# Kernel optimization log

Measured on AMD Instinct MI355X. Metric: run time of the kernel, lower is better.

Reference implementation:

```python
import jax, jax.numpy as jnp
import numpy as np

V, D, DFF, L, H, N, K, NB, R = 32000, 512, 2048, 4, 8, 64, 8, 32, 64
B, S = 2, 512
DH = D // H


def _layernorm(x, g, b, eps=1e-5):
    m = x.mean(-1, keepdims=True)
    v = ((x - m) ** 2).mean(-1, keepdims=True)
    return (x - m) * jax.lax.rsqrt(v + eps) * g + b


def _forward(input_ids, token_emb, pos_emb, basis_A, basis_emb, recipe,
             Wq, bq, Wk, bk, Wv, bv, Ws, bs, Wup, bup, Wdown, bdown,
             ln1_g, ln1_b, ln2_g, ln2_b, alpha, lnf_g, lnf_b):
    Bc, Sc = input_ids.shape
    x = token_emb[input_ids] + pos_emb[:Sc][None]          # [B,S,D]
    causal = jnp.tril(jnp.ones((Sc, Sc), dtype=bool))
    neg = jnp.asarray(-jnp.inf, x.dtype)
    scale = jnp.asarray(1.0 / np.sqrt(DH), x.dtype)
    for i in range(L):
        rec = recipe[i]                                    # [N,NB]
        neuron_emb = jax.nn.softmax(rec, -1) @ basis_emb   # [N,D] routing embedding
        # ---- SimpleRouter on norm1(x) ----
        n1 = _layernorm(x, ln1_g[i], ln1_b[i])
        q = (n1 @ Wq[i] + bq[i]).reshape(Bc, Sc, H, DH)
        k = (n1 @ Wk[i] + bk[i]).reshape(Bc, Sc, H, DH)
        v = (n1 @ Wv[i] + bv[i]).reshape(Bc, Sc, H, DH)
        attn = jnp.einsum('bqhd,bkhd->bhqk', q, k) * scale
        attn = jnp.where(causal[None, None], attn, neg)
        attn = jax.nn.softmax(attn, -1)
        ctx = jnp.einsum('bhqk,bkhd->bqhd', attn, v).reshape(Bc, Sc, D)
        query = jnp.concatenate([n1, ctx], -1) @ Ws[i] + bs[i]   # [B,S,D]
        scores = query @ neuron_emb.T                            # [B,S,N]
        topk_scores, topk_idx = jax.lax.top_k(scores, K)
        weights = jax.nn.softmax(topk_scores, -1)                # [B,S,K]
        # ---- BasisResidualFFN on norm2(x) ----
        n2 = _layernorm(x, ln2_g[i], ln2_b[i])
        sel = jax.nn.softmax(rec[topk_idx], -1)                  # [B,S,K,NB]
        token_recipe = (sel * weights[..., None]).sum(2)         # [B,S,NB]
        # delta = x @ W_A @ W_A^T with W_A = token_recipe . basis_A, computed
        # WITHOUT materializing [B,S,D,R] (same math, associativity only)
        proj = jnp.einsum('bsd,ndr->bsnr', n2, basis_A)          # [B,S,NB,R]
        h = jnp.einsum('bsn,bsnr->bsr', token_recipe, proj)      # [B,S,R]
        delta = jnp.einsum('bsn,bsr,ndr->bsd', token_recipe, h, basis_A)
        xf = n2 + alpha[i] * delta
        ff = jax.nn.gelu(xf @ Wup[i] + bup[i], approximate=False) @ Wdown[i] + bdown[i]
        x = x + ff                                               # dropout=0 (eval)
    x = _layernorm(x, lnf_g, lnf_b)
    return x @ token_emb.T                                       # tied head


def setup_inputs() -> dict:
    key = jax.random.key(0)
    ks = iter(jax.random.split(key, 40))
    std = 0.02
    nrm = lambda shape, s=std: jax.random.normal(next(ks), shape, jnp.float32) * s
    input_ids = jax.random.randint(next(ks), (B, S), 0, V)
    basis_A = jax.random.normal(next(ks), (NB, D, R), jnp.float32)
    basis_A = basis_A / jnp.linalg.norm(basis_A.reshape(NB, -1), axis=-1)[:, None, None]
    basis_emb = jax.random.normal(next(ks), (NB, D), jnp.float32)
    basis_emb = basis_emb / jnp.linalg.norm(basis_emb, axis=-1, keepdims=True)
    return dict(
        input_ids=input_ids,
        token_emb=nrm((V, D)), pos_emb=nrm((S, D)),
        basis_A=basis_A, basis_emb=basis_emb,
        recipe=jax.random.normal(next(ks), (L, N, NB), jnp.float32) * 0.5,
        Wq=nrm((L, D, D)), bq=jnp.zeros((L, D)),
        Wk=nrm((L, D, D)), bk=jnp.zeros((L, D)),
        Wv=nrm((L, D, D)), bv=jnp.zeros((L, D)),
        Ws=nrm((L, 2 * D, D)), bs=jnp.zeros((L, D)),
        Wup=nrm((L, D, DFF)), bup=jnp.zeros((L, DFF)),
        Wdown=nrm((L, DFF, D)), bdown=jnp.zeros((L, D)),
        ln1_g=jnp.ones((L, D)), ln1_b=jnp.zeros((L, D)),
        ln2_g=jnp.ones((L, D)), ln2_b=jnp.zeros((L, D)),
        alpha=jnp.full((L,), 0.1, jnp.float32),
        lnf_g=jnp.ones((D,)), lnf_b=jnp.zeros((D,)),
    )


def reference(input_ids, token_emb, pos_emb, basis_A, basis_emb, recipe,
              Wq, bq, Wk, bk, Wv, bv, Ws, bs, Wup, bup, Wdown, bdown,
              ln1_g, ln1_b, ln2_g, ln2_b, alpha, lnf_g, lnf_b):
    return _forward(input_ids, token_emb, pos_emb, basis_A, basis_emb, recipe,
                    Wq, bq, Wk, bk, Wv, bv, Ws, bs, Wup, bup, Wdown, bdown,
                    ln1_g, ln1_b, ln2_g, ln2_b, alpha, lnf_g, lnf_b)
```

## Files before the change

### kernel.cpp

```cpp
#include <hip/hip_runtime.h>
#include <hip/hip_bf16.h>
#include <math.h>

#define V_  32000
#define D_  512
#define DFF_ 2048
#define L_  4
#define H_  8
#define N_  64
#define K_  8
#define NB_ 32
#define R_  64
#define B_  2
#define S_  512
#define T_  1024
#define DH_ 64

typedef short bhalf8 __attribute__((ext_vector_type(8)));
typedef float floatx4 __attribute__((ext_vector_type(4)));

#define GLOAD16(gp, lp) __builtin_amdgcn_global_load_lds( \
    (const __attribute__((address_space(1))) void*)(gp), \
    (__attribute__((address_space(3))) void*)(lp), 16, 0, 0)

__device__ __forceinline__ float gelu_f(float v) {
    return 0.5f * v * (1.0f + erff(v * 0.70710678118654752f));
}

__device__ __forceinline__ unsigned pk2(float a, float b) {
    unsigned ua = (unsigned)__bfloat16_as_ushort(__float2bfloat16(a));
    unsigned ub = (unsigned)__bfloat16_as_ushort(__float2bfloat16(b));
    return ua | (ub << 16);
}

template<int BM, int BN, int WR, int WC, int EPI>
__device__ __forceinline__ void gemm_dev(
    short* __restrict__ lds,
    const __hip_bfloat16* __restrict__ A, int lda, long sA,
    const __hip_bfloat16* __restrict__ Bt, int ldb, long sB,
    const float* __restrict__ bias,
    const float* __restrict__ aux,
    void* __restrict__ Cv, int ldc, long sC,
    int Kdim, int bm, int bn, int z)
{
    constexpr int FM = BM / WR / 16;
    constexpr int FN = BN / WC / 16;
    constexpr int ACH = BM * 8;
    constexpr int BCH = BN * 8;
    constexpr int HALF = (BM + BN) * 64;
    A  += (long)z * sA;
    Bt += (long)z * sB;
    const int tid = threadIdx.x;
    const int w = tid >> 6, lane = tid & 63;
    const int wr = w / WC, wc = w % WC;
    const int moff = wr * (BM / WR), noff = wc * (BN / WC);
    floatx4 acc[FM][FN] = {};

    auto stage = [&](int buf, int k0) {
        char* baseA = (char*)(lds + buf * HALF);
        char* baseB = (char*)(lds + buf * HALF + BM * 64);
        #pragma unroll
        for (int i = 0; i < ACH / 256; i++) {
            int c = tid + i * 256;
            int m = c >> 3, u = (c & 7) ^ (m & 7);
            GLOAD16(A + (long)(bm + m) * lda + k0 + u * 8, baseA + (w * 64 + i * 256) * 16);
        }
        #pragma unroll
        for (int i = 0; i < BCH / 256; i++) {
            int c = tid + i * 256;
            int m = c >> 3, u = (c & 7) ^ (m & 7);
            GLOAD16(Bt + (long)(bn + m) * ldb + k0 + u * 8, baseB + (w * 64 + i * 256) * 16);
        }
    };

    const int nt = Kdim >> 6;
    stage(0, 0);
    __syncthreads();
    int cur = 0;
    for (int t = 0; t < nt; ++t) {
        if (t + 1 < nt) stage(cur ^ 1, (t + 1) * 64);
        const char* baseA = (const char*)(lds + cur * HALF);
        const char* baseB = (const char*)(lds + cur * HALF + BM * 64);
        #pragma unroll
        for (int kk = 0; kk < 2; kk++) {
            bhalf8 af[FM], bf[FN];
            #pragma unroll
            for (int fm = 0; fm < FM; fm++) {
                int row = moff + fm * 16 + (lane & 15);
                int u = (kk * 4 + (lane >> 4)) ^ (row & 7);
                af[fm] = *(const bhalf8*)(baseA + row * 128 + u * 16);
            }
            #pragma unroll
            for (int fn = 0; fn < FN; fn++) {
                int row = noff + fn * 16 + (lane & 15);
                int u = (kk * 4 + (lane >> 4)) ^ (row & 7);
                bf[fn] = *(const bhalf8*)(baseB + row * 128 + u * 16);
            }
            #pragma unroll
            for (int fm = 0; fm < FM; fm++)
                #pragma unroll
                for (int fn = 0; fn < FN; fn++)
                    acc[fm][fn] = __builtin_amdgcn_mfma_f32_16x16x32_bf16(
                        af[fm], bf[fn], acc[fm][fn], 0, 0, 0);
        }
        __syncthreads();
        cur ^= 1;
    }

    float* Cf = (float*)Cv;
    __hip_bfloat16* Cb = (__hip_bfloat16*)Cv;
    __hip_bfloat16* vtb = (EPI == 5) ? (__hip_bfloat16*)(void*)aux : nullptr;
    const long zoff = (long)z * sC;
    const int lr = lane >> 4, lc = lane & 15;

    if constexpr (EPI == 7) {
        float* st = (float*)lds;
        #pragma unroll
        for (int fm = 0; fm < FM; fm++)
            #pragma unroll
            for (int fn = 0; fn < FN; fn++)
                #pragma unroll
                for (int i = 0; i < 4; i++)
                    st[(moff + fm * 16 + lr * 4 + i) * 65 + noff + fn * 16 + lc] =
                        acc[fm][fn][i];
        __syncthreads();
        #pragma unroll
        for (int it = 0; it < (BM * BN / 4) / 256; it++) {
            int slot = it * 256 + tid;
            int r = slot >> 4, c4 = (slot & 15) * 4;
            float4 v = *(float4*)&st[r * 65 + c4];
            *(float4*)&Cf[zoff + (long)(bm + r) * ldc + bn + c4] = v;
        }
        __syncthreads();
        return;
    }

    float alphaV = (EPI == 3) ? bias[0] : 0.f;
    #pragma unroll
    for (int fm = 0; fm < FM; fm++) {
        #pragma unroll
        for (int fn = 0; fn < FN; fn++) {
            int cN = bn + noff + fn * 16 + lc;
            float bv = (EPI == 3 || !bias || (EPI == 6 && z != 0)) ? 0.f : bias[cN];
            #pragma unroll
            for (int i = 0; i < 4; i++) {
                int rM = bm + moff + fm * 16 + lr * 4 + i;
                long idx = zoff + (long)rM * ldc + cN;
                float v = acc[fm][fn][i] + bv;
                if constexpr (EPI == 0) Cf[idx] = v;
                else if constexpr (EPI == 1) Cb[idx] = __float2bfloat16(v);
                else if constexpr (EPI == 2) Cb[idx] = __float2bfloat16(gelu_f(v));
                else if constexpr (EPI == 3)
                    Cb[idx] = __float2bfloat16(aux[idx] + alphaV * acc[fm][fn][i]);
                else if constexpr (EPI == 4) Cf[idx] += v;
                else if constexpr (EPI == 5) {
                    __hip_bfloat16 bvv = __float2bfloat16(v);
                    Cb[idx] = bvv;
                    if (cN >= 1024) {
                        int hh = (cN - 1024) >> 6, dh = (cN - 1024) & 63;
                        int bb = rM >> 9, ss = rM & 511;
                        vtb[(((long)bb * 8 + hh) * 64 + dh) * 512 + ss] = bvv;
                    }
                }
                else if constexpr (EPI == 6) atomicAdd(&Cf[idx], v);
            }
        }
    }
}

template<int BM, int BN, int WR, int WC, int EPI, int SWZ = 0>
__global__ __launch_bounds__(256) void gemm_mfma(
    const __hip_bfloat16* __restrict__ A, int lda, long sA,
    const __hip_bfloat16* __restrict__ Bt, int ldb, long sB,
    const float* __restrict__ bias,
    const float* __restrict__ aux,
    void* __restrict__ Cv, int ldc, long sC,
    int Kdim)
{
    __shared__ short lds[2 * (BM + BN) * 64];
    int bm, bn;
    if constexpr (SWZ == 1) {
        constexpr int MT = T_ / BM;
        constexpr int NP = V_ / BN;
        constexpr int PPX = (NP + 7) / 8;
        int d = blockIdx.x;
        int xcd = d & 7, k = d >> 3;
        int ty = xcd * PPX + (k >> 3);
        if (ty >= NP) return;
        bm = (k & (MT - 1)) * BM;
        bn = ty * BN;
    } else {
        bm = blockIdx.y * BM;
        bn = blockIdx.x * BN;
    }
    gemm_dev<BM, BN, WR, WC, EPI>(lds, A, lda, sA, Bt, ldb, sB, bias, aux,
                                  Cv, ldc, sC, Kdim, bm, bn, blockIdx.z);
}

__global__ __launch_bounds__(256) void mega_gemm(
    const __hip_bfloat16* __restrict__ catB, const __hip_bfloat16* __restrict__ qkvT,
    const float* __restrict__ bqkv, __hip_bfloat16* __restrict__ VtB,
    __hip_bfloat16* __restrict__ qkvB,
    const __hip_bfloat16* __restrict__ WsB, const __hip_bfloat16* __restrict__ neB,
    __hip_bfloat16* __restrict__ WsneK,
    const __hip_bfloat16* __restrict__ n2B, const __hip_bfloat16* __restrict__ projT,
    float* __restrict__ P)
{
    __shared__ short lds[2 * 192 * 64];
    int blk = blockIdx.x;
    if (blk < 384) {
        gemm_dev<64, 64, 2, 2, 5>(lds, catB, 1024, 0, qkvT, D_, 0, bqkv,
                                  (const float*)VtB, qkvB, 1536, 0, D_,
                                  (blk / 24) * 64, (blk % 24) * 64, 0);
    } else if (blk < 400) {
        gemm_dev<64, 64, 2, 2, 1>(lds, WsB, D_, 0, neB, D_, 0, nullptr, nullptr,
                                  WsneK, N_, 0, D_, (blk - 384) * 64, 0, 0);
    } else {
        int local = blk - 400;
        gemm_dev<128, 64, 2, 2, 7>(lds, n2B, D_, 0, projT, D_, (long)R_ * D_,
                                   nullptr, nullptr, P, NB_ * R_, R_, D_,
                                   (local & 7) * 128, 0, local >> 3);
    }
}

__global__ __launch_bounds__(256) void attn_mfma(
    const __hip_bfloat16* __restrict__ qkv,
    const __hip_bfloat16* __restrict__ vt,
    __hip_bfloat16* __restrict__ catB)
{
    __shared__ short pbuf[4][16][72];
    const int tid = threadIdx.x;
    const int w = tid >> 6, lane = tid & 63;
    const int g = lane >> 4, ql = lane & 15;
    const int h = blockIdx.y, b = blockIdx.z;
    const int qbase = blockIdx.x * 64 + w * 16;

    const long qrow = ((long)(b * S_ + qbase + ql)) * 1536 + h * DH_;
    bhalf8 qa0 = *(const bhalf8*)(qkv + qrow + g * 8);
    bhalf8 qa1 = *(const bhalf8*)(qkv + qrow + 32 + g * 8);
    const __hip_bfloat16* kB = qkv + 512;
    const __hip_bfloat16* vbase = vt + ((long)(b * H_ + h)) * DH_ * S_;

    floatx4 o[4] = {};
    float m = -INFINITY, ls = 0.f;
    const float SC = 0.125f * 1.44269504088896f;
    const int nblk = blockIdx.x + 1;

    for (int kvb = 0; kvb < nblk; kvb++) {
        const int kb0 = kvb * 64;
        floatx4 st[4];
        #pragma unroll
        for (int t = 0; t < 4; t++) {
            long krow = ((long)(b * S_ + kb0 + t * 16 + ql)) * 1536 + h * DH_;
            bhalf8 ka0 = *(const bhalf8*)(kB + krow + g * 8);
            bhalf8 ka1 = *(const bhalf8*)(kB + krow + 32 + g * 8);
            floatx4 z = {};
            z = __builtin_amdgcn_mfma_f32_16x16x32_bf16(ka0, qa0, z, 0, 0, 0);
            z = __builtin_amdgcn_mfma_f32_16x16x32_bf16(ka1, qa1, z, 0, 0, 0);
            st[t] = z;
        }
        const int q = qbase + ql;
        float p[4][4];
        float m4 = -INFINITY;
        #pragma unroll
        for (int t = 0; t < 4; t++)
            #pragma unroll
            for (int i = 0; i < 4; i++) {
                int kv = kb0 + t * 16 + g * 4 + i;
                float v = (kv <= q) ? st[t][i] * SC : -INFINITY;
                p[t][i] = v; m4 = fmaxf(m4, v);
            }
        m4 = fmaxf(m4, __shfl_xor(m4, 16));
        m4 = fmaxf(m4, __shfl_xor(m4, 32));
        float mnew = fmaxf(m, m4);
        float corr = exp2f(m - mnew);
        m = mnew;
        float lsum = 0.f;
        #pragma unroll
        for (int t = 0; t < 4; t++)
            #pragma unroll
            for (int i = 0; i < 4; i++) {
                float e = exp2f(p[t][i] - mnew);
                p[t][i] = e; lsum += e;
            }
        lsum += __shfl_xor(lsum, 16);
        lsum += __shfl_xor(lsum, 32);
        ls = ls * corr + lsum;
        unsigned* prow = (unsigned*)&pbuf[w][ql][0];
        #pragma unroll
        for (int t = 0; t < 4; t++) {
            prow[t * 8 + g * 2]     = pk2(p[t][0], p[t][1]);
            prow[t * 8 + g * 2 + 1] = pk2(p[t][2], p[t][3]);
        }
        #pragma unroll
        for (int i = 0; i < 4; i++) {
            float c = __shfl(corr, g * 4 + i);
            #pragma unroll
            for (int dt = 0; dt < 4; dt++) o[dt][i] *= c;
        }
        __syncthreads();
        #pragma unroll
        for (int ks = 0; ks < 2; ks++) {
            bhalf8 pa = *(const bhalf8*)&pbuf[w][ql][ks * 32 + g * 8];
            #pragma unroll
            for (int dt = 0; dt < 4; dt++) {
                bhalf8 vb = *(const bhalf8*)(vbase + (long)(dt * 16 + ql) * S_ + kb0 + ks * 32 + g * 8);
                o[dt] = __builtin_amdgcn_mfma_f32_16x16x32_bf16(pa, vb, o[dt], 0, 0, 0);
            }
        }
        __syncthreads();
    }
    const float inv = 1.f / ls;
    #pragma unroll
    for (int i = 0; i < 4; i++) {
        float iv = __shfl(inv, g * 4 + i);
        int trow = b * S_ + qbase + g * 4 + i;
        #pragma unroll
        for (int dt = 0; dt < 4; dt++)
            catB[(long)trow * 1024 + 512 + h * DH_ + dt * 16 + ql] =
                __float2bfloat16(o[dt][i] * iv);
    }
}

__device__ __forceinline__ void tcvt_dev(const float* in, int ldn, long sIn,
                                         __hip_bfloat16* out, int ldk, long sOut,
                                         int bx, int by, int bz, float (*tsh)[33]) {
    in  += (long)bz * sIn;
    out += (long)bz * sOut;
    int k0 = by * 32, n0 = bx * 32;
    int tx = threadIdx.x & 31, ty = threadIdx.x >> 5;
    #pragma unroll
    for (int r = 0; r < 4; r++) tsh[ty * 4 + r][tx] = in[(long)(k0 + ty * 4 + r) * ldn + n0 + tx];
    __syncthreads();
    #pragma unroll
    for (int r = 0; r < 4; r++)
        out[(long)(n0 + ty * 4 + r) * ldk + k0 + tx] = __float2bfloat16(tsh[tx][ty * 4 + r]);
}

__device__ __forceinline__ void cvt8(const float* in, __hip_bfloat16* out, long i) {
    float4 v0 = *(const float4*)(in + i);
    float4 v1 = *(const float4*)(in + i + 4);
    uint4 pkv = make_uint4(pk2(v0.x, v0.y), pk2(v0.z, v0.w),
                           pk2(v1.x, v1.y), pk2(v1.z, v1.w));
    *(uint4*)(out + i) = pkv;
}

__global__ __launch_bounds__(256) void prologue_kernel(
    const float* __restrict__ temb, __hip_bfloat16* __restrict__ tembB,
    const float* __restrict__ basisA, __hip_bfloat16* __restrict__ projT,
    __hip_bfloat16* __restrict__ deltaT,
    const float* __restrict__ bq, const float* __restrict__ bk,
    const float* __restrict__ bv, float* __restrict__ bqkv,
    const float* __restrict__ Wq, const float* __restrict__ Wk,
    const float* __restrict__ Wv, __hip_bfloat16* __restrict__ qkvT,
    const float* __restrict__ Wup, __hip_bfloat16* __restrict__ WupT,
    const float* __restrict__ Wdn, __hip_bfloat16* __restrict__ WdnT,
    const float* __restrict__ Ws, __hip_bfloat16* __restrict__ WsB,
    const int* __restrict__ ids, const float* __restrict__ pemb,
    float* __restrict__ x)
{
    __shared__ float tsh[32][33];
    const int blk = blockIdx.x, tid = threadIdx.x;
    if (blk < 8000) {
        cvt8(temb, tembB, ((long)blk * 256 + tid) * 8);
    } else if (blk < 12096) {
        long i = (long)(blk - 8000) * 256 + tid;
        int r = i & 63; int d = (i >> 6) & 511; int n = i >> 15;
        __hip_bfloat16 v = __float2bfloat16(basisA[i]);
        projT[((long)n * R_ + r) * D_ + d] = v;
        deltaT[(long)d * (NB_ * R_) + n * R_ + r] = v;
    } else if (blk < 12120) {
        int i = (blk - 12096) * 256 + tid;
        int l = i / 1536, j = i % 1536;
        float v = (j < 512) ? bq[l * 512 + j] : (j < 1024) ? bk[l * 512 + j - 512]
                                                           : bv[l * 512 + j - 1024];
        bqkv[i] = v;
    } else if (blk < 13144) {
        int lin = blk - 12120;
        tcvt_dev(Wq, D_, (long)D_ * D_, qkvT, D_, (long)1536 * D_,
                 lin & 15, (lin >> 4) & 15, lin >> 8, tsh);
    } else if (blk < 14168) {
        int lin = blk - 13144;
        tcvt_dev(Wk, D_, (long)D_ * D_, qkvT + 512 * 512, D_, (long)1536 * D_,
                 lin & 15, (lin >> 4) & 15, lin >> 8, tsh);
    } else if (blk < 15192) {
        int lin = blk - 14168;
        tcvt_dev(Wv, D_, (long)D_ * D_, qkvT + 1024 * 512, D_, (long)1536 * D_,
                 lin & 15, (lin >> 4) & 15, lin >> 8, tsh);
    } else if (blk < 19288) {
        int lin = blk - 15192;
        tcvt_dev(Wup, DFF_, (long)D_ * DFF_, WupT, D_, (long)D_ * DFF_,
                 lin & 63, (lin >> 6) & 15, lin >> 10, tsh);
    } else if (blk < 23384) {
        int lin = blk - 19288;
        tcvt_dev(Wdn, D_, (long)DFF_ * D_, WdnT, DFF_, (long)DFF_ * D_,
                 lin & 15, (lin >> 4) & 63, lin >> 10, tsh);
    } else if (blk < 24408) {
        cvt8(Ws, WsB, ((long)(blk - 23384) * 256 + tid) * 8);
    } else {
        int t = blk - 24408;
        int s = t % S_;
        int id = ids[t];
        for (int d = tid; d < D_; d += 256)
            x[(long)t * D_ + d] = temb[(long)id * D_ + d] + pemb[(long)s * D_ + d];
    }
}

__device__ __forceinline__ float wave_sum(float v) {
    #pragma unroll
    for (int off = 1; off < 64; off <<= 1) v += __shfl_xor(v, off);
    return v;
}

__device__ __forceinline__ void ln_wave(const float* __restrict__ row,
                                        const float* __restrict__ g,
                                        const float* __restrict__ b,
                                        float* __restrict__ outf,
                                        __hip_bfloat16* __restrict__ outb,
                                        int ldo, long t) {
    int lane = threadIdx.x & 63;
    float4 a0 = *(const float4*)(row + lane * 8);
    float4 a1 = *(const float4*)(row + lane * 8 + 4);
    float v[8] = {a0.x, a0.y, a0.z, a0.w, a1.x, a1.y, a1.z, a1.w};
    float s = 0.f;
    #pragma unroll
    for (int j = 0; j < 8; j++) s += v[j];
    float mean = wave_sum(s) * (1.0f / D_);
    float vs = 0.f;
    #pragma unroll
    for (int j = 0; j < 8; j++) { v[j] -= mean; vs += v[j] * v[j]; }
    float rstd = rsqrtf(wave_sum(vs) * (1.0f / D_) + 1e-5f);
    float4 g0 = *(const float4*)(g + lane * 8), g1 = *(const float4*)(g + lane * 8 + 4);
    float4 b0 = *(const float4*)(b + lane * 8), b1 = *(const float4*)(b + lane * 8 + 4);
    float gg[8] = {g0.x, g0.y, g0.z, g0.w, g1.x, g1.y, g1.z, g1.w};
    float bb[8] = {b0.x, b0.y, b0.z, b0.w, b1.x, b1.y, b1.z, b1.w};
    float o[8];
    #pragma unroll
    for (int j = 0; j < 8; j++) o[j] = v[j] * rstd * gg[j] + bb[j];
    if (outf) {
        *(float4*)(outf + t * D_ + lane * 8)     = make_float4(o[0], o[1], o[2], o[3]);
        *(float4*)(outf + t * D_ + lane * 8 + 4) = make_float4(o[4], o[5], o[6], o[7]);
    }
    uint4 pkv = make_uint4(pk2(o[0], o[1]), pk2(o[2], o[3]), pk2(o[4], o[5]), pk2(o[6], o[7]));
    *(uint4*)(outb + (long)t * ldo + lane * 8) = pkv;
}

__global__ __launch_bounds__(256) void prep_kernel(
    const float* __restrict__ x,
    const float* __restrict__ ln1g, const float* __restrict__ ln1b,
    const float* __restrict__ ln2g, const float* __restrict__ ln2b,
    const float* __restrict__ rec, const float* __restrict__ bemb,
    const float* __restrict__ bs,
    __hip_bfloat16* __restrict__ catB, float* __restrict__ buf1,
    __hip_bfloat16* __restrict__ n2B,
    __hip_bfloat16* __restrict__ neb, float* __restrict__ sel,
    float* __restrict__ bsne)
{
    int blk = blockIdx.x, tid = threadIdx.x, w = tid >> 6;
    if (blk < 256) {
        long t = blk * 4 + w;
        ln_wave(x + t * D_, ln1g, ln1b, nullptr, catB, 1024, t);
    } else if (blk < 512) {
        long t = (blk - 256) * 4 + w;
        ln_wave(x + t * D_, ln2g, ln2b, buf1, n2B, 512, t);
    } else {
        __shared__ float red[256];
        __shared__ float wsm[NB_];
        int n = blk - 512;
        if (tid == 0) {
            float mx = -1e30f;
            for (int i = 0; i < NB_; i++) mx = fmaxf(mx, rec[n * NB_ + i]);
            float sm = 0.f;
            for (int i = 0; i < NB_; i++) { float e = expf(rec[n * NB_ + i] - mx); wsm[i] = e; sm += e; }
            float inv = 1.f / sm;
            for (int i = 0; i < NB_; i++) wsm[i] *= inv;
        }
        __syncthreads();
        if (tid < NB_) sel[n * NB_ + tid] = wsm[tid];
        float part = 0.f;
        for (int d = tid; d < D_; d += 256) {
            float acc = 0.f;
            #pragma unroll
            for (int nb = 0; nb < NB_; nb++) acc += wsm[nb] * bemb[nb * D_ + d];
            neb[(long)n * D_ + d] = __float2bfloat16(acc);
            part += bs[d] * acc;
        }
        red[tid] = part; __syncthreads();
        for (int off = 128; off; off >>= 1) { if (tid < off) red[tid] += red[tid + off]; __syncthreads(); }
        if (tid == 0) bsne[n] = red[0];
    }
}

__global__ __launch_bounds__(256) void ln_kernel(const float* __restrict__ in,
                                                 const float* __restrict__ g,
                                                 const float* __restrict__ b,
                                                 __hip_bfloat16* __restrict__ outb) {
    long t = blockIdx.x * 4 + (threadIdx.x >> 6);
    ln_wave(in + t * D_, g, b, nullptr, outb, 512, t);
}

__global__ __launch_bounds__(256) void route_hg(
    const __hip_bfloat16* __restrict__ catB, const __hip_bfloat16* __restrict__ WsneK,
    const float* __restrict__ bsne, const float* __restrict__ sel,
    const float* __restrict__ P, __hip_bfloat16* __restrict__ g)
{
    int t = blockIdx.x, tid = threadIdx.x;
    __shared__ float catf[1024];
    __shared__ float part[4][64];
    __shared__ float trl[32];
    __shared__ float hl[64];
    {
        short4 vv = *(const short4*)(catB + (long)t * 1024 + tid * 4);
        catf[tid * 4 + 0] = __bfloat162float(*(__hip_bfloat16*)&vv.x);
        catf[tid * 4 + 1] = __bfloat162float(*(__hip_bfloat16*)&vv.y);
        catf[tid * 4 + 2] = __bfloat162float(*(__hip_bfloat16*)&vv.z);
        catf[tid * 4 + 3] = __bfloat162float(*(__hip_bfloat16*)&vv.w);
    }
    __syncthreads();
    int n = tid & 63, q = tid >> 6;
    {
        const __hip_bfloat16* wp = WsneK + (long)q * 256 * 64 + n;
        const float* cf = catf + q * 256;
        float a0 = 0.f, a1 = 0.f, a2 = 0.f, a3 = 0.f;
        #pragma unroll 16
        for (int j = 0; j < 256; j += 4) {
            a0 = fmaf(cf[j],     __bfloat162float(wp[(j)     * 64]), a0);
            a1 = fmaf(cf[j + 1], __bfloat162float(wp[(j + 1) * 64]), a1);
            a2 = fmaf(cf[j + 2], __bfloat162float(wp[(j + 2) * 64]), a2);
            a3 = fmaf(cf[j + 3], __bfloat162float(wp[(j + 3) * 64]), a3);
        }
        part[q][n] = (a0 + a1) + (a2 + a3);
    }
    __syncthreads();
    if (tid < 64) {
        int lane = tid;
        float myval = part[0][lane] + part[1][lane] + part[2][lane] + part[3][lane] + bsne[lane];
        float topv[K_]; int topi[K_];
        #pragma unroll
        for (int kk = 0; kk < K_; kk++) {
            float v = myval; int idx = lane;
            #pragma unroll
            for (int off = 32; off; off >>= 1) {
                float ov = __shfl_down(v, off);
                int oi = __shfl_down(idx, off);
                if (ov > v || (ov == v && oi < idx)) { v = ov; idx = oi; }
            }
            v = __shfl(v, 0); idx = __shfl(idx, 0);
            topv[kk] = v; topi[kk] = idx;
            if (lane == idx) myval = -INFINITY;
        }
        float mx = topv[0];
        float wgt[K_], sum = 0.f;
        #pragma unroll
        for (int kk = 0; kk < K_; kk++) { wgt[kk] = expf(topv[kk] - mx); sum += wgt[kk]; }
        float inv = 1.f / sum;
        if (lane < NB_) {
            float a = 0.f;
            #pragma unroll
            for (int kk = 0; kk < K_; kk++) a += wgt[kk] * inv * sel[topi[kk] * NB_ + lane];
            trl[lane] = a;
        }
    }
    __syncthreads();
    if (tid < 64) {
        float acc = 0.f;
        const float* p = P + (long)t * 2048 + tid;
        #pragma unroll
        for (int nn = 0; nn < 32; nn++) acc += trl[nn] * p[nn * 64];
        hl[tid] = acc;
    }
    __syncthreads();
    #pragma unroll
    for (int j = 0; j < 8; j++) {
        int idx = tid * 8 + j;
        int nn = idx >> 6, r = idx & 63;
        g[(long)t * 2048 + idx] = __float2bfloat16(trl[nn] * hl[r]);
    }
}

extern "C" void kernel_launch(void* const* d_in, const int* in_sizes, int n_in,
                              void* d_out, int out_size, void* d_ws, size_t ws_size,
                              hipStream_t stream) {
    const int*   ids    = (const int*)d_in[0];
    const float* temb   = (const float*)d_in[1];
    const float* pemb   = (const float*)d_in[2];
    const float* basisA = (const float*)d_in[3];
    const float* bemb   = (const float*)d_in[4];
    const float* recipe = (const float*)d_in[5];
    const float* Wq = (const float*)d_in[6],  *bq = (const float*)d_in[7];
    const float* Wk = (const float*)d_in[8],  *bk = (const float*)d_in[9];
    const float* Wv = (const float*)d_in[10], *bv = (const float*)d_in[11];
    const float* Ws = (const float*)d_in[12], *bs = (const float*)d_in[13];
    const float* Wup = (const float*)d_in[14], *bup = (const float*)d_in[15];
    const float* Wdn = (const float*)d_in[16], *bdn = (const float*)d_in[17];
    const float* ln1g = (const float*)d_in[18], *ln1b = (const float*)d_in[19];
    const float* ln2g = (const float*)d_in[20], *ln2b = (const float*)d_in[21];
    const float* alpha = (const float*)d_in[22];
    const float* lnfg = (const float*)d_in[23], *lnfb = (const float*)d_in[24];
    float* out = (float*)d_out;
    float* W = (float*)d_ws;

    float* x    = W + 0;
    float* buf1 = W + 524288;
    float* bsne = W + 1114112;
    float* sel  = W + 1212416;
    float* P    = W + 1214464;
    float* bqkv = W + 3835904;
    __hip_bfloat16* SB = (__hip_bfloat16*)(W + 3844096);
    __hip_bfloat16* tembB  = SB + 0;
    __hip_bfloat16* qkvT   = SB + 16384000;
    __hip_bfloat16* WsB    = SB + 19529728;
    __hip_bfloat16* WupT   = SB + 21626880;
    __hip_bfloat16* WdnT   = SB + 25821184;
    __hip_bfloat16* projT  = SB + 30015488;
    __hip_bfloat16* deltaT = SB + 31064064;
    __hip_bfloat16* neB    = SB + 32112640;
    __hip_bfloat16* catB   = SB + 32145408;
    __hip_bfloat16* WsneK  = SB + 33193984;
    __hip_bfloat16* n2B    = SB + 33718272;
    __hip_bfloat16* xfB    = SB + 34242560;
    __hip_bfloat16* gB     = SB + 34766848;
    __hip_bfloat16* ffhB   = SB + 36864000;
    __hip_bfloat16* qkvB   = SB + 38961152;
    __hip_bfloat16* VtB    = SB + 40534016;

    dim3 blk(256);
    prologue_kernel<<<25432, blk, 0, stream>>>(
        temb, tembB, basisA, projT, deltaT, bq, bk, bv, bqkv,
        Wq, Wk, Wv, qkvT, Wup, WupT, Wdn, WdnT, Ws, WsB, ids, pemb, x);

    for (int l = 0; l < L_; l++) {
        prep_kernel<<<576, blk, 0, stream>>>(
            x, ln1g + l * D_, ln1b + l * D_, ln2g + l * D_, ln2b + l * D_,
            recipe + (long)l * N_ * NB_, bemb, bs + l * D_,
            catB, buf1, n2B, neB, sel, bsne);
        mega_gemm<<<656, blk, 0, stream>>>(
            catB, qkvT + (long)l * 1536 * 512, bqkv + l * 1536, VtB, qkvB,
            WsB + (long)l * 1024 * 512, neB, WsneK, n2B, projT, P);
        attn_mfma<<<dim3(8, H_, B_), blk, 0, stream>>>(qkvB, VtB, catB);
        route_hg<<<T_, blk, 0, stream>>>(catB, WsneK, bsne, sel, P, gB);
        gemm_mfma<32, 64, 1, 4, 3><<<dim3(8, 32), blk, 0, stream>>>(
            gB, NB_ * R_, 0, deltaT, NB_ * R_, 0, alpha + l, buf1,
            xfB, D_, 0, NB_ * R_);
        gemm_mfma<64, 64, 2, 2, 2><<<dim3(32, 16), blk, 0, stream>>>(
            xfB, D_, 0, WupT + (long)l * D_ * DFF_, D_, 0, bup + l * DFF_, nullptr,
            ffhB, DFF_, 0, D_);
        gemm_mfma<32, 64, 1, 4, 6><<<dim3(8, 32, 2), blk, 0, stream>>>(
            ffhB, DFF_, 1024, WdnT + (long)l * DFF_ * D_, DFF_, 1024, bdn + l * D_, nullptr,
            x, D_, 0, 1024);
    }
    ln_kernel<<<256, blk, 0, stream>>>(x, lnfg, lnfb, n2B);
    gemm_mfma<128, 64, 2, 2, 7, 1><<<dim3(4032), blk, 0, stream>>>(
        n2B, D_, 0, tembB, D_, 0, nullptr, nullptr, out, V_, 0, D_);
}
```

Measured before the change: 534.2 us.

## Enlarge GEMM tiles, store P in bf16, and stage epilogue writes through LDS

The LM-head GEMM moves from 128x64 to 128x128 tiles (2048 blocks), and the EPI 7 epilogue is reworked to stage half the tile at a time through a padded LDS buffer so it fits. The basis projection P becomes bf16 with a new coalesced bf16 LDS-staged epilogue (EPI 8/9), and the FFN up GEMM uses 64x128 tiles with that epilogue. The delta and down GEMMs grow to 64x64 tiles. The aim is more reuse per block and less output bandwidth, at the cost of fewer blocks, more register pressure and lower precision for P.

```diff
diff --git a/kernel.cpp b/kernel.cpp
--- a/kernel.cpp
+++ b/kernel.cpp
@@ -115,23 +115,64 @@
 
     if constexpr (EPI == 7) {
         float* st = (float*)lds;
-        #pragma unroll
-        for (int fm = 0; fm < FM; fm++)
-            #pragma unroll
-            for (int fn = 0; fn < FN; fn++)
+        constexpr int STR = BN + 4;
+        #pragma unroll
+        for (int h = 0; h < 2; h++) {
+            __syncthreads();
+            #pragma unroll
+            for (int fm = 0; fm < FM; fm++) {
+                int rowbase = moff + fm * 16;
+                if (((rowbase >> 5) & 1) != h) continue;
+                int crow0 = (rowbase & 31) + ((rowbase >> 6) << 5);
                 #pragma unroll
-                for (int i = 0; i < 4; i++)
-                    st[(moff + fm * 16 + lr * 4 + i) * 65 + noff + fn * 16 + lc] =
-                        acc[fm][fn][i];
+                for (int fn = 0; fn < FN; fn++) {
+                    int col = noff + fn * 16 + lc;
+                    #pragma unroll
+                    for (int i = 0; i < 4; i++)
+                        st[(crow0 + lr * 4 + i) * STR + col] = acc[fm][fn][i];
+                }
+            }
+            __syncthreads();
+            constexpr int ITERS = (BM / 2) * BN / 4 / 256;
+            #pragma unroll
+            for (int it = 0; it < ITERS; it++) {
+                int slot = it * 256 + tid;
+                int crow = slot / (BN / 4), c4 = (slot % (BN / 4)) * 4;
+                int r = (crow & 31) + ((crow >> 5) << 6) + h * 32;
+                *(float4*)&Cf[zoff + (long)(bm + r) * ldc + bn + c4] =
+                    *(float4*)&st[crow * STR + c4];
+            }
+        }
+        return;
+    }
+    if constexpr (EPI == 8 || EPI == 9) {
+        short* sh = lds;
+        constexpr int STR = BN + 8;
         __syncthreads();
         #pragma unroll
-        for (int it = 0; it < (BM * BN / 4) / 256; it++) {
+        for (int fm = 0; fm < FM; fm++) {
+            #pragma unroll
+            for (int fn = 0; fn < FN; fn++) {
+                int col = noff + fn * 16 + lc;
+                float bv = bias ? bias[bn + col] : 0.f;
+                #pragma unroll
+                for (int i = 0; i < 4; i++) {
+                    float v = acc[fm][fn][i] + bv;
+                    if (EPI == 9) v = gelu_f(v);
+                    sh[(moff + fm * 16 + lr * 4 + i) * STR + col] =
+                        __bfloat16_as_short(__float2bfloat16(v));
+                }
+            }
+        }
+        __syncthreads();
+        constexpr int ITERS = BM * BN / 8 / 256;
+        #pragma unroll
+        for (int it = 0; it < ITERS; it++) {
             int slot = it * 256 + tid;
-            int r = slot >> 4, c4 = (slot & 15) * 4;
-            float4 v = *(float4*)&st[r * 65 + c4];
-            *(float4*)&Cf[zoff + (long)(bm + r) * ldc + bn + c4] = v;
-        }
-        __syncthreads();
+            int r = slot / (BN / 8), c8 = (slot % (BN / 8)) * 8;
+            *(uint4*)&Cb[zoff + (long)(bm + r) * ldc + bn + c8] =
+                *(uint4*)&sh[r * STR + c8];
+        }
         return;
     }
 
@@ -185,9 +226,9 @@
         constexpr int PPX = (NP + 7) / 8;
         int d = blockIdx.x;
         int xcd = d & 7, k = d >> 3;
-        int ty = xcd * PPX + (k >> 3);
+        int ty = xcd * PPX + k / MT;
         if (ty >= NP) return;
-        bm = (k & (MT - 1)) * BM;
+        bm = (k % MT) * BM;
         bn = ty * BN;
     } else {
         bm = blockIdx.y * BM;
@@ -204,7 +245,7 @@
     const __hip_bfloat16* __restrict__ WsB, const __hip_bfloat16* __restrict__ neB,
     __hip_bfloat16* __restrict__ WsneK,
     const __hip_bfloat16* __restrict__ n2B, const __hip_bfloat16* __restrict__ projT,
-    float* __restrict__ P)
+    __hip_bfloat16* __restrict__ Pb)
 {
     __shared__ short lds[2 * 192 * 64];
     int blk = blockIdx.x;
@@ -217,8 +258,8 @@
                                   WsneK, N_, 0, D_, (blk - 384) * 64, 0, 0);
     } else {
         int local = blk - 400;
-        gemm_dev<128, 64, 2, 2, 7>(lds, n2B, D_, 0, projT, D_, (long)R_ * D_,
-                                   nullptr, nullptr, P, NB_ * R_, R_, D_,
+        gemm_dev<128, 64, 2, 2, 8>(lds, n2B, D_, 0, projT, D_, (long)R_ * D_,
+                                   nullptr, nullptr, Pb, NB_ * R_, R_, D_,
                                    (local & 7) * 128, 0, local >> 3);
     }
 }
@@ -502,7 +543,7 @@
 __global__ __launch_bounds__(256) void route_hg(
     const __hip_bfloat16* __restrict__ catB, const __hip_bfloat16* __restrict__ WsneK,
     const float* __restrict__ bsne, const float* __restrict__ sel,
-    const float* __restrict__ P, __hip_bfloat16* __restrict__ g)
+    const __hip_bfloat16* __restrict__ Pb, __hip_bfloat16* __restrict__ g)
 {
     int t = blockIdx.x, tid = threadIdx.x;
     __shared__ float catf[1024];
@@ -564,9 +605,9 @@
     __syncthreads();
     if (tid < 64) {
         float acc = 0.f;
-        const float* p = P + (long)t * 2048 + tid;
-        #pragma unroll
-        for (int nn = 0; nn < 32; nn++) acc += trl[nn] * p[nn * 64];
+        const __hip_bfloat16* p = Pb + (long)t * 2048 + tid;
+        #pragma unroll
+        for (int nn = 0; nn < 32; nn++) acc += trl[nn] * __bfloat162float(p[nn * 64]);
         hl[tid] = acc;
     }
     __syncthreads();
@@ -604,7 +645,6 @@
     float* buf1 = W + 524288;
     float* bsne = W + 1114112;
     float* sel  = W + 1212416;
-    float* P    = W + 1214464;
     float* bqkv = W + 3835904;
     __hip_bfloat16* SB = (__hip_bfloat16*)(W + 3844096);
     __hip_bfloat16* tembB  = SB + 0;
@@ -623,6 +663,7 @@
     __hip_bfloat16* ffhB   = SB + 36864000;
     __hip_bfloat16* qkvB   = SB + 38961152;
     __hip_bfloat16* VtB    = SB + 40534016;
+    __hip_bfloat16* Pb     = SB + 41058304;
 
     dim3 blk(256);
     prologue_kernel<<<25432, blk, 0, stream>>>(
@@ -636,20 +677,20 @@
             catB, buf1, n2B, neB, sel, bsne);
         mega_gemm<<<656, blk, 0, stream>>>(
             catB, qkvT + (long)l * 1536 * 512, bqkv + l * 1536, VtB, qkvB,
-            WsB + (long)l * 1024 * 512, neB, WsneK, n2B, projT, P);
+            WsB + (long)l * 1024 * 512, neB, WsneK, n2B, projT, Pb);
         attn_mfma<<<dim3(8, H_, B_), blk, 0, stream>>>(qkvB, VtB, catB);
-        route_hg<<<T_, blk, 0, stream>>>(catB, WsneK, bsne, sel, P, gB);
-        gemm_mfma<32, 64, 1, 4, 3><<<dim3(8, 32), blk, 0, stream>>>(
+        route_hg<<<T_, blk, 0, stream>>>(catB, WsneK, bsne, sel, Pb, gB);
+        gemm_mfma<64, 64, 2, 2, 3><<<dim3(8, 16), blk, 0, stream>>>(
             gB, NB_ * R_, 0, deltaT, NB_ * R_, 0, alpha + l, buf1,
             xfB, D_, 0, NB_ * R_);
-        gemm_mfma<64, 64, 2, 2, 2><<<dim3(32, 16), blk, 0, stream>>>(
+        gemm_mfma<64, 128, 2, 2, 9><<<dim3(16, 16), blk, 0, stream>>>(
             xfB, D_, 0, WupT + (long)l * D_ * DFF_, D_, 0, bup + l * DFF_, nullptr,
             ffhB, DFF_, 0, D_);
-        gemm_mfma<32, 64, 1, 4, 6><<<dim3(8, 32, 2), blk, 0, stream>>>(
+        gemm_mfma<64, 64, 2, 2, 6><<<dim3(8, 16, 2), blk, 0, stream>>>(
             ffhB, DFF_, 1024, WdnT + (long)l * DFF_ * D_, DFF_, 1024, bdn + l * D_, nullptr,
             x, D_, 0, 1024);
     }
     ln_kernel<<<256, blk, 0, stream>>>(x, lnfg, lnfb, n2B);
-    gemm_mfma<128, 64, 2, 2, 7, 1><<<dim3(4032), blk, 0, stream>>>(
+    gemm_mfma<128, 128, 2, 2, 7, 1><<<dim3(2048), blk, 0, stream>>>(
         n2B, D_, 0, tembB, D_, 0, nullptr, nullptr, out, V_, 0, D_);
 }
```

Result: slower. 545.9 us (+2.2%).
